# Kernel tuning notes

Hardware: AMD Instinct MI355X
Metric: run time of the kernel (lower is better)

## Reference

```python
import jax, jax.numpy as jnp
import numpy as np

NEG_SLOPE = 0.2   # PyG GATConv leaky_relu default
BN_EPS = 1e-5


def setup_inputs() -> dict:
    key = jax.random.key(0)
    ks = jax.random.split(key, 6)
    B, C, N, T = 8, 128, 64, 512   # batch, in_channels, electrodes, time_steps
    H, D = 4, 32                   # heads, per-head dim; OUT = H*D = 128
    E = 256                        # knn edges (k=4 per electrode)
    OUT = H * D
    x = jax.random.normal(ks[0], (B, C, N, T), dtype=jnp.float32)
    W = jax.random.normal(ks[1], (C, H, D), dtype=jnp.float32) / np.float32(np.sqrt(C))
    att_src = jax.random.normal(ks[2], (H, D), dtype=jnp.float32) / np.float32(np.sqrt(D))
    att_dst = jax.random.normal(ks[3], (H, D), dtype=jnp.float32) / np.float32(np.sqrt(D))
    bias = jnp.zeros((OUT,), dtype=jnp.float32)
    bn_gamma = jnp.ones((OUT,), jnp.float32)
    bn_beta = jnp.zeros((OUT,), jnp.float32)
    bn_mean = jnp.zeros((OUT,), jnp.float32)   # BatchNorm running stats (eval mode)
    bn_var = jnp.ones((OUT,), jnp.float32)
    edge_index = jax.random.randint(ks[4], (2, E), 0, N, dtype=jnp.int32)
    return dict(x=x, W=W, att_src=att_src, att_dst=att_dst, bias=bias,
                bn_gamma=bn_gamma, bn_beta=bn_beta, bn_mean=bn_mean,
                bn_var=bn_var, edge_index=edge_index)


def _gat(x, W, att_src, att_dst, bias, edge_index):
    # x: [BT, N, C]; fixed graph shared across all BT slices -> fully batched
    BT, N, C = x.shape
    H, D = att_src.shape
    loops = jnp.arange(N, dtype=edge_index.dtype)
    src = jnp.concatenate([edge_index[0], loops])   # GATConv add_self_loops=True
    dst = jnp.concatenate([edge_index[1], loops])   # [E']
    h = jnp.einsum('bnc,chd->bnhd', x, W)           # [BT,N,H,D]
    a_src = jnp.einsum('bnhd,hd->bnh', h, att_src)  # [BT,N,H]
    a_dst = jnp.einsum('bnhd,hd->bnh', h, att_dst)
    scores = jax.nn.leaky_relu(a_src[:, src] + a_dst[:, dst], NEG_SLOPE)  # [BT,E',H]
    scores_e = jnp.transpose(scores, (1, 0, 2))                           # [E',BT,H]
    # segment softmax over incoming edges of each target node
    m = jax.ops.segment_max(scores_e, dst, num_segments=N)               # [N,BT,H]
    ex = jnp.exp(scores_e - m[dst])
    denom = jax.ops.segment_sum(ex, dst, num_segments=N)
    alpha = ex / denom[dst]                                               # [E',BT,H]
    msgs = alpha[..., None] * jnp.transpose(h[:, src], (1, 0, 2, 3))      # [E',BT,H,D]
    agg = jax.ops.segment_sum(msgs, dst, num_segments=N)                  # [N,BT,H,D]
    out = jnp.transpose(agg, (1, 0, 2, 3)).reshape(BT, N, H * D) + bias   # concat heads
    return out


def reference(x, W, att_src, att_dst, bias, bn_gamma, bn_beta, bn_mean, bn_var, edge_index):
    B, C, N, T = x.shape
    xt = jnp.transpose(x, (0, 3, 2, 1)).reshape(B * T, N, C)  # loop dim batched
    g = _gat(xt, W, att_src, att_dst, bias, edge_index)        # [BT,N,OUT]
    g = g.mean(axis=1)                                         # mean over nodes -> [BT,OUT]
    OUT = g.shape[-1]
    g = g.reshape(B, T, OUT).transpose(0, 2, 1)                # [B,OUT,T]
    y = (g - bn_mean[:, None]) * jax.lax.rsqrt(bn_var[:, None] + BN_EPS) \
        * bn_gamma[:, None] + bn_beta[:, None]                 # BatchNorm1d (eval)
    return y[:, :, None, :]                                    # [B,OUT,1,T]
```

## Files before the change

### kernel.cpp

```cpp
#include <hip/hip_runtime.h>
#include <math.h>

#define B_ 8
#define C_ 128
#define N_ 64
#define T_ 512
#define H_ 4
#define D_ 32
#define OUT_ 128
#define E_ 256
#define EP_ 320
#define NEG_SLOPE 0.2f
#define BN_EPS 1e-5f
#define TC 16
#define NT_ (N_ * T_)

__global__ void setup_kernel(const float* __restrict__ W,
                             const float* __restrict__ att_src,
                             const float* __restrict__ att_dst,
                             const int* __restrict__ edge_index,
                             float* __restrict__ wa,
                             int* __restrict__ iOff_g, int* __restrict__ iSrc_g,
                             int* __restrict__ oOff_g, int* __restrict__ oDst_g) {
  __shared__ int icnt[N_], ibase[N_ + 1], ifill[N_];
  __shared__ int ocnt[N_], obase[N_ + 1], ofill[N_];
  __shared__ int esrc[EP_], edst[EP_];
  int tid = threadIdx.x;

  for (int idx = tid; idx < C_ * 8; idx += blockDim.x) {
    int c = idx >> 3, j = idx & 7, h = j & 3;
    const float* att = (j < 4) ? att_src : att_dst;
    float s = 0.f;
    for (int d = 0; d < D_; ++d)
      s += W[(c * H_ + h) * D_ + d] * att[h * D_ + d];
    wa[idx] = s;
  }
  if (tid < N_) { icnt[tid] = 0; ifill[tid] = 0; ocnt[tid] = 0; ofill[tid] = 0; }
  __syncthreads();
  for (int e = tid; e < EP_; e += blockDim.x) {
    int s, d;
    if (e < E_) { s = edge_index[e]; d = edge_index[E_ + e]; }
    else        { s = e - E_;        d = e - E_; }
    esrc[e] = s; edst[e] = d;
    atomicAdd(&icnt[d], 1);
    atomicAdd(&ocnt[s], 1);
  }
  __syncthreads();
  if (tid == 0) {
    int ai = 0, ao = 0;
    for (int n = 0; n < N_; ++n) {
      ibase[n] = ai; ai += icnt[n];
      obase[n] = ao; ao += ocnt[n];
    }
    ibase[N_] = ai; obase[N_] = ao;
  }
  __syncthreads();
  if (tid <= N_) { iOff_g[tid] = ibase[tid]; oOff_g[tid] = obase[tid]; }
  for (int e = tid; e < EP_; e += blockDim.x) {
    int s = esrc[e], d = edst[e];
    int pi = ibase[d] + atomicAdd(&ifill[d], 1);
    iSrc_g[pi] = s;
    int po = obase[s] + atomicAdd(&ofill[s], 1);
    oDst_g[po] = d;
  }
}

__global__ __launch_bounds__(1024, 1)
void mega_kernel(const float* __restrict__ x,
                 const float* __restrict__ wa_g,
                 const float* __restrict__ Wm,
                 const int* __restrict__ iOff_g, const int* __restrict__ iSrc_g,
                 const int* __restrict__ oOff_g, const int* __restrict__ oDst_g,
                 const float* __restrict__ bias,
                 const float* __restrict__ bn_gamma,
                 const float* __restrict__ bn_beta,
                 const float* __restrict__ bn_mean,
                 const float* __restrict__ bn_var,
                 float* __restrict__ out) {
  __shared__ __align__(16) char arena[114688];
  float* a_l   = (float*)arena;
  float4* redA = (float4*)(arena + 40960);
  float4* redB = (float4*)(arena + 73728);
  float* z_l   = (float*)(arena + 40960);
  float* w_l   = (float*)(arena + 57344);
  float* wstage= (float*)(arena + 40960);
  float* wal   = (float*)(arena + 106496);
  int* iSrc = (int*)(arena + 110592);
  int* oDst = iSrc + EP_;
  int* iOff = oDst + EP_;
  int* oOff = iOff + (N_ + 1);

  const int tid = threadIdx.x;
  const int b = blockIdx.x & 7;
  const int tchunk = blockIdx.x >> 3;
  const int t0 = tchunk * TC;

  if (tid < EP_) { iSrc[tid] = iSrc_g[tid]; oDst[tid] = oDst_g[tid]; }
  if (tid >= EP_ && tid < EP_ + N_ + 1) {
    int i = tid - EP_;
    iOff[i] = iOff_g[i]; oOff[i] = oOff_g[i];
  }
  if (tid < C_ * 8) wal[tid] = wa_g[tid];
  __syncthreads();

  {
    const int q  = tid & 3;
    const int cq = (tid >> 2) & 3;
    const int n1 = tid >> 4;
    const float* xp = x + ((size_t)(b * C_ + cq * 32) * N_ + n1) * T_ + t0 + q * 4;
    float4 acc[8];
#pragma unroll
    for (int j = 0; j < 8; ++j) { acc[j].x = 0.f; acc[j].y = 0.f; acc[j].z = 0.f; acc[j].w = 0.f; }
    for (int kb = 0; kb < 4; ++kb) {
      float4 xv[8];
#pragma unroll
      for (int u = 0; u < 8; ++u)
        xv[u] = *reinterpret_cast<const float4*>(xp + (size_t)(kb * 8 + u) * NT_);
#pragma unroll
      for (int u = 0; u < 8; ++u) {
        const int c = cq * 32 + kb * 8 + u;
        const float4 w0 = *reinterpret_cast<const float4*>(&wal[c * 8]);
        const float4 w1 = *reinterpret_cast<const float4*>(&wal[c * 8 + 4]);
        const float4 xu = xv[u];
        acc[0].x = fmaf(xu.x, w0.x, acc[0].x); acc[0].y = fmaf(xu.y, w0.x, acc[0].y);
        acc[0].z = fmaf(xu.z, w0.x, acc[0].z); acc[0].w = fmaf(xu.w, w0.x, acc[0].w);
        acc[1].x = fmaf(xu.x, w0.y, acc[1].x); acc[1].y = fmaf(xu.y, w0.y, acc[1].y);
        acc[1].z = fmaf(xu.z, w0.y, acc[1].z); acc[1].w = fmaf(xu.w, w0.y, acc[1].w);
        acc[2].x = fmaf(xu.x, w0.z, acc[2].x); acc[2].y = fmaf(xu.y, w0.z, acc[2].y);
        acc[2].z = fmaf(xu.z, w0.z, acc[2].z); acc[2].w = fmaf(xu.w, w0.z, acc[2].w);
        acc[3].x = fmaf(xu.x, w0.w, acc[3].x); acc[3].y = fmaf(xu.y, w0.w, acc[3].y);
        acc[3].z = fmaf(xu.z, w0.w, acc[3].z); acc[3].w = fmaf(xu.w, w0.w, acc[3].w);
        acc[4].x = fmaf(xu.x, w1.x, acc[4].x); acc[4].y = fmaf(xu.y, w1.x, acc[4].y);
        acc[4].z = fmaf(xu.z, w1.x, acc[4].z); acc[4].w = fmaf(xu.w, w1.x, acc[4].w);
        acc[5].x = fmaf(xu.x, w1.y, acc[5].x); acc[5].y = fmaf(xu.y, w1.y, acc[5].y);
        acc[5].z = fmaf(xu.z, w1.y, acc[5].z); acc[5].w = fmaf(xu.w, w1.y, acc[5].w);
        acc[6].x = fmaf(xu.x, w1.z, acc[6].x); acc[6].y = fmaf(xu.y, w1.z, acc[6].y);
        acc[6].z = fmaf(xu.z, w1.z, acc[6].z); acc[6].w = fmaf(xu.w, w1.z, acc[6].w);
        acc[7].x = fmaf(xu.x, w1.w, acc[7].x); acc[7].y = fmaf(xu.y, w1.w, acc[7].y);
        acc[7].z = fmaf(xu.z, w1.w, acc[7].z); acc[7].w = fmaf(xu.w, w1.w, acc[7].w);
      }
    }
    if (cq == 1) {
#pragma unroll
      for (int j = 0; j < 8; ++j) redA[(j * 64 + n1) * 4 + q] = acc[j];
    } else if (cq == 3) {
#pragma unroll
      for (int j = 0; j < 8; ++j) redB[(j * 64 + n1) * 4 + q] = acc[j];
    }
    __syncthreads();
    if (cq == 0) {
#pragma unroll
      for (int j = 0; j < 8; ++j) {
        float4 o = redA[(j * 64 + n1) * 4 + q];
        acc[j].x += o.x; acc[j].y += o.y; acc[j].z += o.z; acc[j].w += o.w;
      }
    } else if (cq == 2) {
#pragma unroll
      for (int j = 0; j < 8; ++j) {
        float4 o = redB[(j * 64 + n1) * 4 + q];
        acc[j].x += o.x; acc[j].y += o.y; acc[j].z += o.z; acc[j].w += o.w;
        redB[(j * 64 + n1) * 4 + q] = acc[j];
      }
    }
    __syncthreads();
    if (cq == 0) {
#pragma unroll
      for (int j = 0; j < 8; ++j) {
        float4 o = redB[(j * 64 + n1) * 4 + q];
        float4 r;
        r.x = acc[j].x + o.x; r.y = acc[j].y + o.y;
        r.z = acc[j].z + o.z; r.w = acc[j].w + o.w;
        *reinterpret_cast<float4*>(&a_l[j * 1280 + n1 * 20 + q * 4]) = r;
      }
    }
    __syncthreads();
  }

  {
    const int t = tid & 15, nd = tid >> 4;
    int e0 = iOff[nd], e1 = iOff[nd + 1];
    float ad0 = a_l[4 * 1280 + nd * 20 + t];
    float ad1 = a_l[5 * 1280 + nd * 20 + t];
    float ad2 = a_l[6 * 1280 + nd * 20 + t];
    float ad3 = a_l[7 * 1280 + nd * 20 + t];
    float m0 = -1e30f, m1 = -1e30f, m2 = -1e30f, m3 = -1e30f;
    for (int e = e0; e < e1; ++e) {
      int s = iSrc[e];
      float v0 = a_l[0 * 1280 + s * 20 + t] + ad0; v0 = v0 > 0.f ? v0 : NEG_SLOPE * v0;
      float v1 = a_l[1 * 1280 + s * 20 + t] + ad1; v1 = v1 > 0.f ? v1 : NEG_SLOPE * v1;
      float v2 = a_l[2 * 1280 + s * 20 + t] + ad2; v2 = v2 > 0.f ? v2 : NEG_SLOPE * v2;
      float v3 = a_l[3 * 1280 + s * 20 + t] + ad3; v3 = v3 > 0.f ? v3 : NEG_SLOPE * v3;
      m0 = fmaxf(m0, v0); m1 = fmaxf(m1, v1);
      m2 = fmaxf(m2, v2); m3 = fmaxf(m3, v3);
    }
    float d0 = 0.f, d1 = 0.f, d2 = 0.f, d3 = 0.f;
    for (int e = e0; e < e1; ++e) {
      int s = iSrc[e];
      float v0 = a_l[0 * 1280 + s * 20 + t] + ad0; v0 = v0 > 0.f ? v0 : NEG_SLOPE * v0;
      float v1 = a_l[1 * 1280 + s * 20 + t] + ad1; v1 = v1 > 0.f ? v1 : NEG_SLOPE * v1;
      float v2 = a_l[2 * 1280 + s * 20 + t] + ad2; v2 = v2 > 0.f ? v2 : NEG_SLOPE * v2;
      float v3 = a_l[3 * 1280 + s * 20 + t] + ad3; v3 = v3 > 0.f ? v3 : NEG_SLOPE * v3;
      d0 += __expf(v0 - m0); d1 += __expf(v1 - m1);
      d2 += __expf(v2 - m2); d3 += __expf(v3 - m3);
    }
    float4 zv;
    zv.x = __expf(-m0) / (d0 * (float)N_);
    zv.y = __expf(-m1) / (d1 * (float)N_);
    zv.z = __expf(-m2) / (d2 * (float)N_);
    zv.w = __expf(-m3) / (d3 * (float)N_);
    __syncthreads();
    *reinterpret_cast<float4*>(&z_l[(nd * 16 + t) * 4]) = zv;
  }
  __syncthreads();

  {
    const int t = tid & 15, src = tid >> 4;
    int e0 = oOff[src], e1 = oOff[src + 1];
    float as0 = a_l[0 * 1280 + src * 20 + t];
    float as1 = a_l[1 * 1280 + src * 20 + t];
    float as2 = a_l[2 * 1280 + src * 20 + t];
    float as3 = a_l[3 * 1280 + src * 20 + t];
    float w0 = 0.f, w1 = 0.f, w2 = 0.f, w3 = 0.f;
    for (int e = e0; e < e1; ++e) {
      int d = oDst[e];
      float4 zv = *reinterpret_cast<const float4*>(&z_l[(d * 16 + t) * 4]);
      float v0 = as0 + a_l[4 * 1280 + d * 20 + t]; v0 = v0 > 0.f ? v0 : NEG_SLOPE * v0;
      float v1 = as1 + a_l[5 * 1280 + d * 20 + t]; v1 = v1 > 0.f ? v1 : NEG_SLOPE * v1;
      float v2 = as2 + a_l[6 * 1280 + d * 20 + t]; v2 = v2 > 0.f ? v2 : NEG_SLOPE * v2;
      float v3 = as3 + a_l[7 * 1280 + d * 20 + t]; v3 = v3 > 0.f ? v3 : NEG_SLOPE * v3;
      w0 += __expf(v0) * zv.x;
      w1 += __expf(v1) * zv.y;
      w2 += __expf(v2) * zv.z;
      w3 += __expf(v3) * zv.w;
    }
    w_l[src * 64 +  0 + t] = w0;
    w_l[src * 64 + 16 + t] = w1;
    w_l[src * 64 + 32 + t] = w2;
    w_l[src * 64 + 48 + t] = w3;
  }
  __syncthreads();

  {
    const int t2 = tid & 15, cl = tid >> 4;
    const float* xA = x + ((size_t)(b * C_ + cl) * N_) * T_ + t0 + t2;
    const float* xB = xA + (size_t)64 * NT_;
    float yrA[4] = {0.f, 0.f, 0.f, 0.f};
    float yrB[4] = {0.f, 0.f, 0.f, 0.f};
    for (int nb = 0; nb < 8; ++nb) {
      float xa[8], xb_[8];
#pragma unroll
      for (int u = 0; u < 8; ++u) {
        xa[u]  = xA[(size_t)(nb * 8 + u) * T_];
        xb_[u] = xB[(size_t)(nb * 8 + u) * T_];
      }
#pragma unroll
      for (int u = 0; u < 8; ++u) {
        const int n = nb * 8 + u;
        float w0 = w_l[n * 64 +  0 + t2];
        float w1 = w_l[n * 64 + 16 + t2];
        float w2 = w_l[n * 64 + 32 + t2];
        float w3 = w_l[n * 64 + 48 + t2];
        yrA[0] = fmaf(xa[u], w0, yrA[0]); yrA[1] = fmaf(xa[u], w1, yrA[1]);
        yrA[2] = fmaf(xa[u], w2, yrA[2]); yrA[3] = fmaf(xa[u], w3, yrA[3]);
        yrB[0] = fmaf(xb_[u], w0, yrB[0]); yrB[1] = fmaf(xb_[u], w1, yrB[1]);
        yrB[2] = fmaf(xb_[u], w2, yrB[2]); yrB[3] = fmaf(xb_[u], w3, yrB[3]);
      }
    }
    float* y_l = a_l;
#pragma unroll
    for (int h = 0; h < 4; ++h) {
      y_l[h * 2176 + cl * 17 + t2]        = yrA[h];
      y_l[h * 2176 + (cl + 64) * 17 + t2] = yrB[h];
    }
  }
  __syncthreads();

  {
    const float4* Wm4 = reinterpret_cast<const float4*>(Wm);
    float4* ws4 = reinterpret_cast<float4*>(wstage);
#pragma unroll
    for (int r = 0; r < 4; ++r) ws4[r * 1024 + tid] = Wm4[r * 1024 + tid];
  }
  __syncthreads();
  {
    const int t3 = tid & 15;
    const int g = tid >> 4;
    const int h = g >> 4;
    const int dp = g & 15;
    const float* y_l = a_l;
    float acc0 = 0.f, acc1 = 0.f;
#pragma unroll 8
    for (int c = 0; c < C_; ++c) {
      float yv = y_l[h * 2176 + c * 17 + t3];
      const float2 wv = *reinterpret_cast<const float2*>(
          &wstage[(c * H_ + h) * D_ + dp * 2]);
      acc0 = fmaf(yv, wv.x, acc0);
      acc1 = fmaf(yv, wv.y, acc1);
    }
    int oc = h * D_ + dp * 2;
    float s0 = bn_gamma[oc] * rsqrtf(bn_var[oc] + BN_EPS);
    float s1 = bn_gamma[oc + 1] * rsqrtf(bn_var[oc + 1] + BN_EPS);
    out[((size_t)b * OUT_ + oc) * T_ + t0 + t3] =
        (acc0 + bias[oc]) * s0 + bn_beta[oc] - bn_mean[oc] * s0;
    out[((size_t)b * OUT_ + oc + 1) * T_ + t0 + t3] =
        (acc1 + bias[oc + 1]) * s1 + bn_beta[oc + 1] - bn_mean[oc + 1] * s1;
  }
}

extern "C" void kernel_launch(void* const* d_in, const int* in_sizes, int n_in,
                              void* d_out, int out_size, void* d_ws, size_t ws_size,
                              hipStream_t stream) {
  const float* x        = (const float*)d_in[0];
  const float* W        = (const float*)d_in[1];
  const float* att_src  = (const float*)d_in[2];
  const float* att_dst  = (const float*)d_in[3];
  const float* bias     = (const float*)d_in[4];
  const float* bn_gamma = (const float*)d_in[5];
  const float* bn_beta  = (const float*)d_in[6];
  const float* bn_mean  = (const float*)d_in[7];
  const float* bn_var   = (const float*)d_in[8];
  const int* edge_index = (const int*)d_in[9];
  float* out = (float*)d_out;

  char* ws = (char*)d_ws;
  float* wa   = (float*)ws;
  int* iOff_g = (int*)(ws + 4096);
  int* iSrc_g = (int*)(ws + 4608);
  int* oOff_g = (int*)(ws + 6144);
  int* oDst_g = (int*)(ws + 6656);

  setup_kernel<<<1, 256, 0, stream>>>(W, att_src, att_dst, edge_index, wa,
                                      iOff_g, iSrc_g, oOff_g, oDst_g);
  mega_kernel<<<256, 1024, 0, stream>>>(x, wa, W, iOff_g, iSrc_g, oOff_g, oDst_g,
                                        bias, bn_gamma, bn_beta, bn_mean, bn_var,
                                        out);
}
```

Before: 73.30 us.

## Split mega kernel into projection and aggregation passes with bf16 x staging

The single fused kernel is split into a projection kernel and an aggregation kernel. The projection kernel computes the attention logits into a workspace and at the same time writes a bf16, tile-transposed copy of x. The aggregation kernel then reads that half-size copy instead of rereading fp32 x, and streams W from global memory instead of staging it in shared memory. This aims to improve occupancy and coalescing and to cut the second read of x. In exchange it adds a workspace round trip (about 32MB of bf16 writes plus reads) and bf16 rounding of x in the weighted sum.

```diff
diff --git a/kernel.cpp b/kernel.cpp
--- a/kernel.cpp
+++ b/kernel.cpp
@@ -12,8 +12,16 @@
 #define EP_ 320
 #define NEG_SLOPE 0.2f
 #define BN_EPS 1e-5f
-#define TC 16
 #define NT_ (N_ * T_)
+
+__device__ inline unsigned short f2bf(float f) {
+  unsigned u = __float_as_uint(f);
+  u += 0x7FFFu + ((u >> 16) & 1u);
+  return (unsigned short)(u >> 16);
+}
+__device__ inline float bf2f(unsigned short s) {
+  return __uint_as_float(((unsigned)s) << 16);
+}
 
 __global__ void setup_kernel(const float* __restrict__ W,
                              const float* __restrict__ att_src,
@@ -65,245 +73,257 @@
   }
 }
 
-__global__ __launch_bounds__(1024, 1)
-void mega_kernel(const float* __restrict__ x,
+__global__ __launch_bounds__(256, 4)
+void proj_kernel(const float* __restrict__ x,
                  const float* __restrict__ wa_g,
-                 const float* __restrict__ Wm,
-                 const int* __restrict__ iOff_g, const int* __restrict__ iSrc_g,
-                 const int* __restrict__ oOff_g, const int* __restrict__ oDst_g,
-                 const float* __restrict__ bias,
-                 const float* __restrict__ bn_gamma,
-                 const float* __restrict__ bn_beta,
-                 const float* __restrict__ bn_mean,
-                 const float* __restrict__ bn_var,
-                 float* __restrict__ out) {
-  __shared__ __align__(16) char arena[114688];
-  float* a_l   = (float*)arena;
-  float4* redA = (float4*)(arena + 40960);
-  float4* redB = (float4*)(arena + 73728);
-  float* z_l   = (float*)(arena + 40960);
-  float* w_l   = (float*)(arena + 57344);
-  float* wstage= (float*)(arena + 40960);
-  float* wal   = (float*)(arena + 106496);
-  int* iSrc = (int*)(arena + 110592);
+                 float* __restrict__ a_ws,
+                 unsigned short* __restrict__ xs) {
+  __shared__ float wal[C_ * 8];
+  __shared__ float4 red4[4 * 8 * 64];
+  const int tid = threadIdx.x;
+  const int bid = blockIdx.x;
+  const int b = bid & 7;
+  const int n = (bid >> 3) & 63;
+  const int th = bid >> 9;
+
+  for (int i = tid; i < C_ * 8; i += 256) wal[i] = wa_g[i];
+  __syncthreads();
+
+  const int cg = tid >> 6, tq = tid & 63;
+  const int tc = th * 16 + (tq >> 2);
+  const int tl = (tq & 3) * 4;
+  const float* xp = x + ((size_t)(b * C_) * N_ + n) * T_ + th * 256 + tq * 4;
+  unsigned short* xsb = xs + ((size_t)(b * 32 + tc) * 128) * 1024 + n * 16 + tl;
+
+  float4 acc[8];
+#pragma unroll
+  for (int j = 0; j < 8; ++j) { acc[j].x = 0.f; acc[j].y = 0.f; acc[j].z = 0.f; acc[j].w = 0.f; }
+  for (int kb = 0; kb < 8; ++kb) {
+    float4 xv[4];
+#pragma unroll
+    for (int u = 0; u < 4; ++u) {
+      int c = cg + (kb * 4 + u) * 4;
+      xv[u] = *reinterpret_cast<const float4*>(xp + (size_t)c * NT_);
+    }
+#pragma unroll
+    for (int u = 0; u < 4; ++u) {
+      int c = cg + (kb * 4 + u) * 4;
+      ushort4 s;
+      s.x = f2bf(xv[u].x); s.y = f2bf(xv[u].y);
+      s.z = f2bf(xv[u].z); s.w = f2bf(xv[u].w);
+      *reinterpret_cast<ushort4*>(xsb + (size_t)c * 1024) = s;
+#pragma unroll
+      for (int j = 0; j < 8; ++j) {
+        float wj = wal[c * 8 + j];
+        acc[j].x = fmaf(xv[u].x, wj, acc[j].x);
+        acc[j].y = fmaf(xv[u].y, wj, acc[j].y);
+        acc[j].z = fmaf(xv[u].z, wj, acc[j].z);
+        acc[j].w = fmaf(xv[u].w, wj, acc[j].w);
+      }
+    }
+  }
+#pragma unroll
+  for (int j = 0; j < 8; ++j) red4[(cg * 8 + j) * 64 + tq] = acc[j];
+  __syncthreads();
+
+#pragma unroll
+  for (int rep = 0; rep < 2; ++rep) {
+    int ss = tid + rep * 256;
+    int j = ss >> 6, tq2 = ss & 63;
+    float4 v0 = red4[(0 * 8 + j) * 64 + tq2];
+    float4 v1 = red4[(1 * 8 + j) * 64 + tq2];
+    float4 v2 = red4[(2 * 8 + j) * 64 + tq2];
+    float4 v3 = red4[(3 * 8 + j) * 64 + tq2];
+    float4 r;
+    r.x = (v0.x + v1.x) + (v2.x + v3.x);
+    r.y = (v0.y + v1.y) + (v2.y + v3.y);
+    r.z = (v0.z + v1.z) + (v2.z + v3.z);
+    r.w = (v0.w + v1.w) + (v2.w + v3.w);
+    *reinterpret_cast<float4*>(
+        a_ws + ((size_t)(b * N_ + n) * 8 + j) * T_ + th * 256 + tq2 * 4) = r;
+  }
+}
+
+__global__ __launch_bounds__(512, 1)
+void agg_kernel(const unsigned short* __restrict__ xs,
+                const float* __restrict__ a_ws,
+                const float* __restrict__ Wm,
+                const int* __restrict__ iOff_g, const int* __restrict__ iSrc_g,
+                const int* __restrict__ oOff_g, const int* __restrict__ oDst_g,
+                const float* __restrict__ bias,
+                const float* __restrict__ bn_gamma,
+                const float* __restrict__ bn_beta,
+                const float* __restrict__ bn_mean,
+                const float* __restrict__ bn_var,
+                float* __restrict__ out) {
+  __shared__ __align__(16) char arena[76816];
+  float* a_l  = (float*)arena;
+  float* z_l  = (float*)(arena + 40960);
+  float* w_l  = (float*)(arena + 57344);
+  unsigned short* xst = (unsigned short*)arena;
+  float* scr  = (float*)(arena + 32768);
+  float* yoct = (float*)(arena + 36864);
+  int* iSrc = (int*)(arena + 73728);
   int* oDst = iSrc + EP_;
   int* iOff = oDst + EP_;
   int* oOff = iOff + (N_ + 1);
 
   const int tid = threadIdx.x;
-  const int b = blockIdx.x & 7;
-  const int tchunk = blockIdx.x >> 3;
-  const int t0 = tchunk * TC;
+  const int b  = blockIdx.x & 7;
+  const int tc = blockIdx.x >> 3;
+  const int t0 = tc * 16;
 
   if (tid < EP_) { iSrc[tid] = iSrc_g[tid]; oDst[tid] = oDst_g[tid]; }
-  if (tid >= EP_ && tid < EP_ + N_ + 1) {
+  else if (tid < EP_ + N_ + 1) {
     int i = tid - EP_;
     iOff[i] = iOff_g[i]; oOff[i] = oOff_g[i];
   }
-  if (tid < C_ * 8) wal[tid] = wa_g[tid];
-  __syncthreads();
-
   {
-    const int q  = tid & 3;
-    const int cq = (tid >> 2) & 3;
-    const int n1 = tid >> 4;
-    const float* xp = x + ((size_t)(b * C_ + cq * 32) * N_ + n1) * T_ + t0 + q * 4;
-    float4 acc[8];
-#pragma unroll
-    for (int j = 0; j < 8; ++j) { acc[j].x = 0.f; acc[j].y = 0.f; acc[j].z = 0.f; acc[j].w = 0.f; }
-    for (int kb = 0; kb < 4; ++kb) {
-      float4 xv[8];
-#pragma unroll
-      for (int u = 0; u < 8; ++u)
-        xv[u] = *reinterpret_cast<const float4*>(xp + (size_t)(kb * 8 + u) * NT_);
-#pragma unroll
-      for (int u = 0; u < 8; ++u) {
-        const int c = cq * 32 + kb * 8 + u;
-        const float4 w0 = *reinterpret_cast<const float4*>(&wal[c * 8]);
-        const float4 w1 = *reinterpret_cast<const float4*>(&wal[c * 8 + 4]);
-        const float4 xu = xv[u];
-        acc[0].x = fmaf(xu.x, w0.x, acc[0].x); acc[0].y = fmaf(xu.y, w0.x, acc[0].y);
-        acc[0].z = fmaf(xu.z, w0.x, acc[0].z); acc[0].w = fmaf(xu.w, w0.x, acc[0].w);
-        acc[1].x = fmaf(xu.x, w0.y, acc[1].x); acc[1].y = fmaf(xu.y, w0.y, acc[1].y);
-        acc[1].z = fmaf(xu.z, w0.y, acc[1].z); acc[1].w = fmaf(xu.w, w0.y, acc[1].w);
-        acc[2].x = fmaf(xu.x, w0.z, acc[2].x); acc[2].y = fmaf(xu.y, w0.z, acc[2].y);
-        acc[2].z = fmaf(xu.z, w0.z, acc[2].z); acc[2].w = fmaf(xu.w, w0.z, acc[2].w);
-        acc[3].x = fmaf(xu.x, w0.w, acc[3].x); acc[3].y = fmaf(xu.y, w0.w, acc[3].y);
-        acc[3].z = fmaf(xu.z, w0.w, acc[3].z); acc[3].w = fmaf(xu.w, w0.w, acc[3].w);
-        acc[4].x = fmaf(xu.x, w1.x, acc[4].x); acc[4].y = fmaf(xu.y, w1.x, acc[4].y);
-        acc[4].z = fmaf(xu.z, w1.x, acc[4].z); acc[4].w = fmaf(xu.w, w1.x, acc[4].w);
-        acc[5].x = fmaf(xu.x, w1.y, acc[5].x); acc[5].y = fmaf(xu.y, w1.y, acc[5].y);
-        acc[5].z = fmaf(xu.z, w1.y, acc[5].z); acc[5].w = fmaf(xu.w, w1.y, acc[5].w);
-        acc[6].x = fmaf(xu.x, w1.z, acc[6].x); acc[6].y = fmaf(xu.y, w1.z, acc[6].y);
-        acc[6].z = fmaf(xu.z, w1.z, acc[6].z); acc[6].w = fmaf(xu.w, w1.z, acc[6].w);
-        acc[7].x = fmaf(xu.x, w1.w, acc[7].x); acc[7].y = fmaf(xu.y, w1.w, acc[7].y);
-        acc[7].z = fmaf(xu.z, w1.w, acc[7].z); acc[7].w = fmaf(xu.w, w1.w, acc[7].w);
-      }
-    }
-    if (cq == 1) {
-#pragma unroll
-      for (int j = 0; j < 8; ++j) redA[(j * 64 + n1) * 4 + q] = acc[j];
-    } else if (cq == 3) {
-#pragma unroll
-      for (int j = 0; j < 8; ++j) redB[(j * 64 + n1) * 4 + q] = acc[j];
+    int n = tid >> 3, j = tid & 7;
+    const float4* src = reinterpret_cast<const float4*>(
+        a_ws + (((size_t)b * N_ + n) * 8 + j) * T_ + t0);
+    float4* dst = reinterpret_cast<float4*>(&a_l[j * 1280 + n * 20]);
+    dst[0] = src[0]; dst[1] = src[1]; dst[2] = src[2]; dst[3] = src[3];
+  }
+  __syncthreads();
+
+  {
+    const int t = tid & 15, g = tid >> 4;
+#pragma unroll
+    for (int rep = 0; rep < 2; ++rep) {
+      int nd = g + rep * 32;
+      int e0 = iOff[nd], e1 = iOff[nd + 1];
+      float ad0 = a_l[4 * 1280 + nd * 20 + t];
+      float ad1 = a_l[5 * 1280 + nd * 20 + t];
+      float ad2 = a_l[6 * 1280 + nd * 20 + t];
+      float ad3 = a_l[7 * 1280 + nd * 20 + t];
+      float m0 = -1e30f, m1 = -1e30f, m2 = -1e30f, m3 = -1e30f;
+      for (int e = e0; e < e1; ++e) {
+        int s = iSrc[e];
+        float v0 = a_l[0 * 1280 + s * 20 + t] + ad0; v0 = v0 > 0.f ? v0 : NEG_SLOPE * v0;
+        float v1 = a_l[1 * 1280 + s * 20 + t] + ad1; v1 = v1 > 0.f ? v1 : NEG_SLOPE * v1;
+        float v2 = a_l[2 * 1280 + s * 20 + t] + ad2; v2 = v2 > 0.f ? v2 : NEG_SLOPE * v2;
+        float v3 = a_l[3 * 1280 + s * 20 + t] + ad3; v3 = v3 > 0.f ? v3 : NEG_SLOPE * v3;
+        m0 = fmaxf(m0, v0); m1 = fmaxf(m1, v1);
+        m2 = fmaxf(m2, v2); m3 = fmaxf(m3, v3);
+      }
+      float d0 = 0.f, d1 = 0.f, d2 = 0.f, d3 = 0.f;
+      for (int e = e0; e < e1; ++e) {
+        int s = iSrc[e];
+        float v0 = a_l[0 * 1280 + s * 20 + t] + ad0; v0 = v0 > 0.f ? v0 : NEG_SLOPE * v0;
+        float v1 = a_l[1 * 1280 + s * 20 + t] + ad1; v1 = v1 > 0.f ? v1 : NEG_SLOPE * v1;
+        float v2 = a_l[2 * 1280 + s * 20 + t] + ad2; v2 = v2 > 0.f ? v2 : NEG_SLOPE * v2;
+        float v3 = a_l[3 * 1280 + s * 20 + t] + ad3; v3 = v3 > 0.f ? v3 : NEG_SLOPE * v3;
+        d0 += __expf(v0 - m0); d1 += __expf(v1 - m1);
+        d2 += __expf(v2 - m2); d3 += __expf(v3 - m3);
+      }
+      float4 zv;
+      zv.x = __expf(-m0) / (d0 * (float)N_);
+      zv.y = __expf(-m1) / (d1 * (float)N_);
+      zv.z = __expf(-m2) / (d2 * (float)N_);
+      zv.w = __expf(-m3) / (d3 * (float)N_);
+      *reinterpret_cast<float4*>(&z_l[(nd * 16 + t) * 4]) = zv;
+    }
+  }
+  __syncthreads();
+
+  {
+    const int t = tid & 15, g = tid >> 4;
+#pragma unroll
+    for (int rep = 0; rep < 2; ++rep) {
+      int src = g + rep * 32;
+      int e0 = oOff[src], e1 = oOff[src + 1];
+      float as0 = a_l[0 * 1280 + src * 20 + t];
+      float as1 = a_l[1 * 1280 + src * 20 + t];
+      float as2 = a_l[2 * 1280 + src * 20 + t];
+      float as3 = a_l[3 * 1280 + src * 20 + t];
+      float w0 = 0.f, w1 = 0.f, w2 = 0.f, w3 = 0.f;
+      for (int e = e0; e < e1; ++e) {
+        int d = oDst[e];
+        float4 zv = *reinterpret_cast<const float4*>(&z_l[(d * 16 + t) * 4]);
+        float v0 = as0 + a_l[4 * 1280 + d * 20 + t]; v0 = v0 > 0.f ? v0 : NEG_SLOPE * v0;
+        float v1 = as1 + a_l[5 * 1280 + d * 20 + t]; v1 = v1 > 0.f ? v1 : NEG_SLOPE * v1;
+        float v2 = as2 + a_l[6 * 1280 + d * 20 + t]; v2 = v2 > 0.f ? v2 : NEG_SLOPE * v2;
+        float v3 = as3 + a_l[7 * 1280 + d * 20 + t]; v3 = v3 > 0.f ? v3 : NEG_SLOPE * v3;
+        w0 += __expf(v0) * zv.x;
+        w1 += __expf(v1) * zv.y;
+        w2 += __expf(v2) * zv.z;
+        w3 += __expf(v3) * zv.w;
+      }
+      w_l[src * 64 +  0 + t] = w0;
+      w_l[src * 64 + 16 + t] = w1;
+      w_l[src * 64 + 32 + t] = w2;
+      w_l[src * 64 + 48 + t] = w3;
+    }
+  }
+  __syncthreads();
+
+  const int cl = tid >> 5;
+  const int tt = (tid >> 1) & 15;
+  const int nh = tid & 1;
+  const int h4 = tid >> 7;
+  const int dp = (tid >> 4) & 7;
+  const int te = tid & 15;
+  float oacc[4] = {0.f, 0.f, 0.f, 0.f};
+  const uint4* xtile = reinterpret_cast<const uint4*>(
+      xs + ((size_t)(b * 32 + tc) * 128) * 1024);
+
+  for (int o = 0; o < 8; ++o) {
+    {
+      const uint4* src = xtile + (size_t)o * 2048;
+      uint4* dst = reinterpret_cast<uint4*>(xst);
+#pragma unroll
+      for (int i = 0; i < 4; ++i) dst[tid + 512 * i] = src[tid + 512 * i];
     }
     __syncthreads();
-    if (cq == 0) {
-#pragma unroll
-      for (int j = 0; j < 8; ++j) {
-        float4 o = redA[(j * 64 + n1) * 4 + q];
-        acc[j].x += o.x; acc[j].y += o.y; acc[j].z += o.z; acc[j].w += o.w;
-      }
-    } else if (cq == 2) {
-#pragma unroll
-      for (int j = 0; j < 8; ++j) {
-        float4 o = redB[(j * 64 + n1) * 4 + q];
-        acc[j].x += o.x; acc[j].y += o.y; acc[j].z += o.z; acc[j].w += o.w;
-        redB[(j * 64 + n1) * 4 + q] = acc[j];
+    {
+      float y0 = 0.f, y1 = 0.f, y2 = 0.f, y3 = 0.f;
+#pragma unroll 8
+      for (int i = 0; i < 32; ++i) {
+        int n = nh * 32 + i;
+        float xv = bf2f(xst[cl * 1024 + n * 16 + tt]);
+        y0 = fmaf(xv, w_l[n * 64 +  0 + tt], y0);
+        y1 = fmaf(xv, w_l[n * 64 + 16 + tt], y1);
+        y2 = fmaf(xv, w_l[n * 64 + 32 + tt], y2);
+        y3 = fmaf(xv, w_l[n * 64 + 48 + tt], y3);
+      }
+      if (nh) {
+        float4 v; v.x = y0; v.y = y1; v.z = y2; v.w = y3;
+        *reinterpret_cast<float4*>(&scr[(cl * 16 + tt) * 4]) = v;
+      }
+      __syncthreads();
+      if (!nh) {
+        float4 v = *reinterpret_cast<const float4*>(&scr[(cl * 16 + tt) * 4]);
+        yoct[0 * 272 + cl * 17 + tt] = y0 + v.x;
+        yoct[1 * 272 + cl * 17 + tt] = y1 + v.y;
+        yoct[2 * 272 + cl * 17 + tt] = y2 + v.z;
+        yoct[3 * 272 + cl * 17 + tt] = y3 + v.w;
       }
     }
     __syncthreads();
-    if (cq == 0) {
-#pragma unroll
-      for (int j = 0; j < 8; ++j) {
-        float4 o = redB[(j * 64 + n1) * 4 + q];
-        float4 r;
-        r.x = acc[j].x + o.x; r.y = acc[j].y + o.y;
-        r.z = acc[j].z + o.z; r.w = acc[j].w + o.w;
-        *reinterpret_cast<float4*>(&a_l[j * 1280 + n1 * 20 + q * 4]) = r;
+    {
+#pragma unroll 4
+      for (int i = 0; i < 16; ++i) {
+        int c = o * 16 + i;
+        float yv = yoct[h4 * 272 + i * 17 + te];
+        const float4 wv = *reinterpret_cast<const float4*>(
+            &Wm[((size_t)c * H_ + h4) * D_ + dp * 4]);
+        oacc[0] = fmaf(yv, wv.x, oacc[0]);
+        oacc[1] = fmaf(yv, wv.y, oacc[1]);
+        oacc[2] = fmaf(yv, wv.z, oacc[2]);
+        oacc[3] = fmaf(yv, wv.w, oacc[3]);
       }
     }
     __syncthreads();
   }
 
-  {
-    const int t = tid & 15, nd = tid >> 4;
-    int e0 = iOff[nd], e1 = iOff[nd + 1];
-    float ad0 = a_l[4 * 1280 + nd * 20 + t];
-    float ad1 = a_l[5 * 1280 + nd * 20 + t];
-    float ad2 = a_l[6 * 1280 + nd * 20 + t];
-    float ad3 = a_l[7 * 1280 + nd * 20 + t];
-    float m0 = -1e30f, m1 = -1e30f, m2 = -1e30f, m3 = -1e30f;
-    for (int e = e0; e < e1; ++e) {
-      int s = iSrc[e];
-      float v0 = a_l[0 * 1280 + s * 20 + t] + ad0; v0 = v0 > 0.f ? v0 : NEG_SLOPE * v0;
-      float v1 = a_l[1 * 1280 + s * 20 + t] + ad1; v1 = v1 > 0.f ? v1 : NEG_SLOPE * v1;
-      float v2 = a_l[2 * 1280 + s * 20 + t] + ad2; v2 = v2 > 0.f ? v2 : NEG_SLOPE * v2;
-      float v3 = a_l[3 * 1280 + s * 20 + t] + ad3; v3 = v3 > 0.f ? v3 : NEG_SLOPE * v3;
-      m0 = fmaxf(m0, v0); m1 = fmaxf(m1, v1);
-      m2 = fmaxf(m2, v2); m3 = fmaxf(m3, v3);
-    }
-    float d0 = 0.f, d1 = 0.f, d2 = 0.f, d3 = 0.f;
-    for (int e = e0; e < e1; ++e) {
-      int s = iSrc[e];
-      float v0 = a_l[0 * 1280 + s * 20 + t] + ad0; v0 = v0 > 0.f ? v0 : NEG_SLOPE * v0;
-      float v1 = a_l[1 * 1280 + s * 20 + t] + ad1; v1 = v1 > 0.f ? v1 : NEG_SLOPE * v1;
-      float v2 = a_l[2 * 1280 + s * 20 + t] + ad2; v2 = v2 > 0.f ? v2 : NEG_SLOPE * v2;
-      float v3 = a_l[3 * 1280 + s * 20 + t] + ad3; v3 = v3 > 0.f ? v3 : NEG_SLOPE * v3;
-      d0 += __expf(v0 - m0); d1 += __expf(v1 - m1);
-      d2 += __expf(v2 - m2); d3 += __expf(v3 - m3);
-    }
-    float4 zv;
-    zv.x = __expf(-m0) / (d0 * (float)N_);
-    zv.y = __expf(-m1) / (d1 * (float)N_);
-    zv.z = __expf(-m2) / (d2 * (float)N_);
-    zv.w = __expf(-m3) / (d3 * (float)N_);
-    __syncthreads();
-    *reinterpret_cast<float4*>(&z_l[(nd * 16 + t) * 4]) = zv;
-  }
-  __syncthreads();
-
-  {
-    const int t = tid & 15, src = tid >> 4;
-    int e0 = oOff[src], e1 = oOff[src + 1];
-    float as0 = a_l[0 * 1280 + src * 20 + t];
-    float as1 = a_l[1 * 1280 + src * 20 + t];
-    float as2 = a_l[2 * 1280 + src * 20 + t];
-    float as3 = a_l[3 * 1280 + src * 20 + t];
-    float w0 = 0.f, w1 = 0.f, w2 = 0.f, w3 = 0.f;
-    for (int e = e0; e < e1; ++e) {
-      int d = oDst[e];
-      float4 zv = *reinterpret_cast<const float4*>(&z_l[(d * 16 + t) * 4]);
-      float v0 = as0 + a_l[4 * 1280 + d * 20 + t]; v0 = v0 > 0.f ? v0 : NEG_SLOPE * v0;
-      float v1 = as1 + a_l[5 * 1280 + d * 20 + t]; v1 = v1 > 0.f ? v1 : NEG_SLOPE * v1;
-      float v2 = as2 + a_l[6 * 1280 + d * 20 + t]; v2 = v2 > 0.f ? v2 : NEG_SLOPE * v2;
-      float v3 = as3 + a_l[7 * 1280 + d * 20 + t]; v3 = v3 > 0.f ? v3 : NEG_SLOPE * v3;
-      w0 += __expf(v0) * zv.x;
-      w1 += __expf(v1) * zv.y;
-      w2 += __expf(v2) * zv.z;
-      w3 += __expf(v3) * zv.w;
-    }
-    w_l[src * 64 +  0 + t] = w0;
-    w_l[src * 64 + 16 + t] = w1;
-    w_l[src * 64 + 32 + t] = w2;
-    w_l[src * 64 + 48 + t] = w3;
-  }
-  __syncthreads();
-
-  {
-    const int t2 = tid & 15, cl = tid >> 4;
-    const float* xA = x + ((size_t)(b * C_ + cl) * N_) * T_ + t0 + t2;
-    const float* xB = xA + (size_t)64 * NT_;
-    float yrA[4] = {0.f, 0.f, 0.f, 0.f};
-    float yrB[4] = {0.f, 0.f, 0.f, 0.f};
-    for (int nb = 0; nb < 8; ++nb) {
-      float xa[8], xb_[8];
-#pragma unroll
-      for (int u = 0; u < 8; ++u) {
-        xa[u]  = xA[(size_t)(nb * 8 + u) * T_];
-        xb_[u] = xB[(size_t)(nb * 8 + u) * T_];
-      }
-#pragma unroll
-      for (int u = 0; u < 8; ++u) {
-        const int n = nb * 8 + u;
-        float w0 = w_l[n * 64 +  0 + t2];
-        float w1 = w_l[n * 64 + 16 + t2];
-        float w2 = w_l[n * 64 + 32 + t2];
-        float w3 = w_l[n * 64 + 48 + t2];
-        yrA[0] = fmaf(xa[u], w0, yrA[0]); yrA[1] = fmaf(xa[u], w1, yrA[1]);
-        yrA[2] = fmaf(xa[u], w2, yrA[2]); yrA[3] = fmaf(xa[u], w3, yrA[3]);
-        yrB[0] = fmaf(xb_[u], w0, yrB[0]); yrB[1] = fmaf(xb_[u], w1, yrB[1]);
-        yrB[2] = fmaf(xb_[u], w2, yrB[2]); yrB[3] = fmaf(xb_[u], w3, yrB[3]);
-      }
-    }
-    float* y_l = a_l;
-#pragma unroll
-    for (int h = 0; h < 4; ++h) {
-      y_l[h * 2176 + cl * 17 + t2]        = yrA[h];
-      y_l[h * 2176 + (cl + 64) * 17 + t2] = yrB[h];
-    }
-  }
-  __syncthreads();
-
-  {
-    const float4* Wm4 = reinterpret_cast<const float4*>(Wm);
-    float4* ws4 = reinterpret_cast<float4*>(wstage);
-#pragma unroll
-    for (int r = 0; r < 4; ++r) ws4[r * 1024 + tid] = Wm4[r * 1024 + tid];
-  }
-  __syncthreads();
-  {
-    const int t3 = tid & 15;
-    const int g = tid >> 4;
-    const int h = g >> 4;
-    const int dp = g & 15;
-    const float* y_l = a_l;
-    float acc0 = 0.f, acc1 = 0.f;
-#pragma unroll 8
-    for (int c = 0; c < C_; ++c) {
-      float yv = y_l[h * 2176 + c * 17 + t3];
-      const float2 wv = *reinterpret_cast<const float2*>(
-          &wstage[(c * H_ + h) * D_ + dp * 2]);
-      acc0 = fmaf(yv, wv.x, acc0);
-      acc1 = fmaf(yv, wv.y, acc1);
-    }
-    int oc = h * D_ + dp * 2;
-    float s0 = bn_gamma[oc] * rsqrtf(bn_var[oc] + BN_EPS);
-    float s1 = bn_gamma[oc + 1] * rsqrtf(bn_var[oc + 1] + BN_EPS);
-    out[((size_t)b * OUT_ + oc) * T_ + t0 + t3] =
-        (acc0 + bias[oc]) * s0 + bn_beta[oc] - bn_mean[oc] * s0;
-    out[((size_t)b * OUT_ + oc + 1) * T_ + t0 + t3] =
-        (acc1 + bias[oc + 1]) * s1 + bn_beta[oc + 1] - bn_mean[oc + 1] * s1;
+#pragma unroll
+  for (int k = 0; k < 4; ++k) {
+    int oc = h4 * D_ + dp * 4 + k;
+    float scale = bn_gamma[oc] * rsqrtf(bn_var[oc] + BN_EPS);
+    float shift = bn_beta[oc] - bn_mean[oc] * scale;
+    out[((size_t)b * OUT_ + oc) * T_ + t0 + te] =
+        (oacc[k] + bias[oc]) * scale + shift;
   }
 }
 
@@ -328,10 +348,13 @@
   int* iSrc_g = (int*)(ws + 4608);
   int* oOff_g = (int*)(ws + 6144);
   int* oDst_g = (int*)(ws + 6656);
+  float* a_ws = (float*)(ws + 16384);
+  unsigned short* xs = (unsigned short*)(ws + 16384 + (size_t)8 * 1024 * 1024);
 
   setup_kernel<<<1, 256, 0, stream>>>(W, att_src, att_dst, edge_index, wa,
                                       iOff_g, iSrc_g, oOff_g, oDst_g);
-  mega_kernel<<<256, 1024, 0, stream>>>(x, wa, W, iOff_g, iSrc_g, oOff_g, oDst_g,
-                                        bias, bn_gamma, bn_beta, bn_mean, bn_var,
-                                        out);
-}
+  proj_kernel<<<1024, 256, 0, stream>>>(x, wa, a_ws, xs);
+  agg_kernel<<<256, 512, 0, stream>>>(xs, a_ws, W, iOff_g, iSrc_g, oOff_g, oDst_g,
+                                      bias, bn_gamma, bn_beta, bn_mean, bn_var,
+                                      out);
+}
```

Measured after the change: 101.3 us. 38.1% more time.
